# Performance work log

Hardware: AMD Instinct MI355X
Metric: run time of the kernel (lower is better)

## Reference

```python
import jax, jax.numpy as jnp
import numpy as np

B, T, D, H = 16, 2048, 512, 512  # batch, seq_len, input_dim, hidden_dim


def setup_inputs() -> dict:
    key = jax.random.key(0)
    k1, k2, k3 = jax.random.split(key, 3)
    x = jax.random.normal(k1, (B, T, D), dtype=jnp.float32)
    # vanilla tanh RnnCell parameters
    W_xh = jax.random.normal(k2, (D, H), dtype=jnp.float32) / np.float32(np.sqrt(D))
    W_hh = jax.random.normal(k3, (H, H), dtype=jnp.float32) / np.float32(np.sqrt(H))
    b = jnp.zeros((H,), dtype=jnp.float32)
    # DFA feedback matrix, 'diagonal' init branch: diag(linspace(0,1,H))
    A = jnp.diag(jnp.linspace(0.0, 1.0, H).astype(jnp.float32))
    return {"x": x, "W_xh": W_xh, "W_hh": W_hh, "b": b, "A": A}


def reference(x, W_xh, W_hh, b, A):
    # Forward of DfaRnn: sequential RNN loop. detach() does not change forward
    # values, so this is a plain tanh RNN scan. A only affects the backward.
    Bb = x.shape[0]
    h0 = jnp.zeros((Bb, W_hh.shape[0]), dtype=x.dtype)

    def step(h, xt):
        h_new = jnp.tanh(xt @ W_xh + h @ W_hh + b)
        return h_new, h_new

    _, hs = jax.lax.scan(step, h0, jnp.swapaxes(x, 0, 1))  # [T,B,H]
    return jnp.swapaxes(hs, 0, 1)  # [B,T,H]
```

## Files before the change

kernel.cpp:

```cpp
#include <hip/hip_runtime.h>
#include <cmath>

#define B_ 16
#define T_ 2048
#define D_ 512
#define H_ 512

__global__ __launch_bounds__(256) void gemm_xw(
    const float* __restrict__ x,
    const float* __restrict__ Wxh,
    const float* __restrict__ bias,
    float* __restrict__ out)
{
    const int tid = threadIdx.x;
    const int n0 = blockIdx.x * 128;
    const int m0 = blockIdx.y * 128;

    __shared__ float As[8][132];
    __shared__ float Bs[8][132];

    const int tx = tid & 15, ty = tid >> 4;
    float acc[8][8] = {};

    const int arow = tid >> 1;
    const int akq  = (tid & 1) * 4;
    const int brow = tid >> 5;
    const int bcol = (tid & 31) * 4;

    for (int k0 = 0; k0 < D_; k0 += 8) {
        float4 a4 = *(const float4*)(x + (size_t)(m0 + arow) * D_ + k0 + akq);
        float4 b4 = *(const float4*)(Wxh + (size_t)(k0 + brow) * H_ + n0 + bcol);
        __syncthreads();
        As[akq + 0][arow] = a4.x;
        As[akq + 1][arow] = a4.y;
        As[akq + 2][arow] = a4.z;
        As[akq + 3][arow] = a4.w;
        *(float4*)(&Bs[brow][bcol]) = b4;
        __syncthreads();
#pragma unroll
        for (int kk = 0; kk < 8; ++kk) {
            float4 a0 = *(const float4*)(&As[kk][ty * 8]);
            float4 a1 = *(const float4*)(&As[kk][ty * 8 + 4]);
            float4 b0 = *(const float4*)(&Bs[kk][tx * 8]);
            float4 b1 = *(const float4*)(&Bs[kk][tx * 8 + 4]);
            float a_[8] = {a0.x, a0.y, a0.z, a0.w, a1.x, a1.y, a1.z, a1.w};
            float b_[8] = {b0.x, b0.y, b0.z, b0.w, b1.x, b1.y, b1.z, b1.w};
#pragma unroll
            for (int i = 0; i < 8; ++i)
#pragma unroll
                for (int j = 0; j < 8; ++j) acc[i][j] += a_[i] * b_[j];
        }
    }

    const float4 bv0 = *(const float4*)(bias + n0 + tx * 8);
    const float4 bv1 = *(const float4*)(bias + n0 + tx * 8 + 4);
    const float bb[8] = {bv0.x, bv0.y, bv0.z, bv0.w, bv1.x, bv1.y, bv1.z, bv1.w};
#pragma unroll
    for (int i = 0; i < 8; ++i) {
        const int m = m0 + ty * 8 + i;
        float4 o0, o1;
        o0.x = acc[i][0] + bb[0]; o0.y = acc[i][1] + bb[1];
        o0.z = acc[i][2] + bb[2]; o0.w = acc[i][3] + bb[3];
        o1.x = acc[i][4] + bb[4]; o1.y = acc[i][5] + bb[5];
        o1.z = acc[i][6] + bb[6]; o1.w = acc[i][7] + bb[7];
        *(float4*)(out + (size_t)m * H_ + n0 + tx * 8)     = o0;
        *(float4*)(out + (size_t)m * H_ + n0 + tx * 8 + 4) = o1;
    }
}

__device__ __forceinline__ void bar_lds() {
    asm volatile("s_waitcnt lgkmcnt(0)\n\ts_barrier" ::: "memory");
}

__global__ __launch_bounds__(512, 2) void rnn_rec(
    const float* __restrict__ Whh,
    float* __restrict__ out,
    unsigned long long* __restrict__ ws)
{
    const int tid = threadIdx.x;
    const int b = blockIdx.x & 15;
    const int s = blockIdx.x >> 4;
    const int j = tid & 63;
    const int p = tid >> 6;
    const int col = (s << 6) + j;

    __shared__ float h_lds[H_];
    __shared__ float part[8 * 64];

    float W_reg[64];
    {
        const float* wbase = Whh + (size_t)(p * 64) * H_ + col;
#pragma unroll
        for (int r = 0; r < 64; ++r) {
            const float* addr = wbase + (size_t)r * H_;
            asm volatile("global_load_dword %0, %1, off"
                         : "=v"(W_reg[r]) : "v"(addr));
        }
        asm volatile("s_waitcnt vmcnt(0)" ::: "memory");
    }

    h_lds[tid] = 0.0f;
    __syncthreads();

    float* outb = out + (size_t)b * T_ * H_;
    unsigned long long* wsb = ws + (size_t)b * 2 * H_;

    float xw0 = 0.0f, xw1 = 0.0f, xw2 = 0.0f;
    if (p == 0) {
        xw0 = outb[(size_t)0 * H_ + col];
        xw1 = outb[(size_t)1 * H_ + col];
        xw2 = outb[(size_t)2 * H_ + col];
    }

    for (int t = 0; t < T_; ++t) {
        float acc = 0.0f;
        const float4* hv = (const float4*)(h_lds + (p << 6));
#pragma unroll
        for (int i = 0; i < 16; ++i) {
            float4 h4 = hv[i];
            acc += h4.x * W_reg[4 * i + 0];
            acc += h4.y * W_reg[4 * i + 1];
            acc += h4.z * W_reg[4 * i + 2];
            acc += h4.w * W_reg[4 * i + 3];
        }
        part[tid] = acc;
        bar_lds();

        const unsigned int tag = (unsigned int)(t + 1);
        const int slot = (t + 1) & 1;
        unsigned long long* wslot = wsb + (size_t)slot * H_;

        if (p == 0) {
            asm volatile("s_waitcnt vmcnt(0)" ::: "memory");
            float ssum = xw0;
#pragma unroll
            for (int q = 0; q < 8; ++q) ssum += part[q * 64 + j];
            union { unsigned int u; float f; } cv;
            cv.f = tanhf(ssum);
            unsigned long long pv =
                ((unsigned long long)tag << 32) | (unsigned long long)cv.u;
            __hip_atomic_store(wslot + col, pv, __ATOMIC_RELAXED,
                               __HIP_MEMORY_SCOPE_AGENT);
            outb[(size_t)t * H_ + col] = cv.f;
            h_lds[col] = cv.f;
            xw0 = xw1;
            xw1 = xw2;
            xw2 = (t + 3 < T_) ? outb[(size_t)(t + 3) * H_ + col] : 0.0f;
        } else {
            const int q = (p == s) ? 0 : p;
            unsigned long long* src = wslot + (q << 6) + j;
            unsigned long long v;
            do {
                v = __hip_atomic_load(src, __ATOMIC_RELAXED,
                                      __HIP_MEMORY_SCOPE_AGENT);
            } while ((unsigned int)(v >> 32) < tag);
            union { unsigned int u; float f; } cv;
            cv.u = (unsigned int)v;
            h_lds[(q << 6) + j] = cv.f;
        }
        bar_lds();
    }
}

extern "C" void kernel_launch(void* const* d_in, const int* in_sizes, int n_in,
                              void* d_out, int out_size, void* d_ws,
                              size_t ws_size, hipStream_t stream) {
    const float* x    = (const float*)d_in[0];
    const float* Wxh  = (const float*)d_in[1];
    const float* Whh  = (const float*)d_in[2];
    const float* bias = (const float*)d_in[3];
    float* out = (float*)d_out;

    hipMemsetAsync(d_ws, 0, (size_t)B_ * 2 * H_ * sizeof(unsigned long long),
                   stream);

    dim3 ggrid(H_ / 128, (B_ * T_) / 128, 1);
    gemm_xw<<<ggrid, 256, 0, stream>>>(x, Wxh, bias, out);

    rnn_rec<<<128, 512, 0, stream>>>(Whh, out, (unsigned long long*)d_ws);
}
```

Measured before the change: 2.973 ms.

## Add same-XCC fast path for cross-block hidden-state exchange via sc0 loads

Blocks record their XCC id in workspace. When producer and consumer slices sit on the same XCC, consumers poll a second mailbox with sc0-scoped loads that can hit the shared L2, and fall back to the agent-scope atomic mailbox on timeout. Producers write both mailboxes. This aims to cut the latency of the per-timestep inter-block handshake, at the cost of an extra store per step, a startup handshake, and reliance on cache-coherence behaviour that differs by scope.

```diff
diff --git a/kernel.cpp b/kernel.cpp
--- a/kernel.cpp
+++ b/kernel.cpp
@@ -68,6 +68,11 @@
     }
 }
 
+#define SLOW_OFF 0
+#define FAST_OFF (B_ * 2 * H_)
+#define HS_OFF   (B_ * 2 * H_ * 2)
+#define WS_U64   (B_ * 2 * H_ * 2 + B_ * 8)
+
 __device__ __forceinline__ void bar_lds() {
     asm volatile("s_waitcnt lgkmcnt(0)\n\ts_barrier" ::: "memory");
 }
@@ -75,7 +80,8 @@
 __global__ __launch_bounds__(512, 2) void rnn_rec(
     const float* __restrict__ Whh,
     float* __restrict__ out,
-    unsigned long long* __restrict__ ws)
+    unsigned long long* __restrict__ ws,
+    int use_fast)
 {
     const int tid = threadIdx.x;
     const int b = blockIdx.x & 15;
@@ -103,7 +109,33 @@
     __syncthreads();
 
     float* outb = out + (size_t)b * T_ * H_;
-    unsigned long long* wsb = ws + (size_t)b * 2 * H_;
+    unsigned long long* wsb_s = ws + SLOW_OFF + (size_t)b * 2 * H_;
+    unsigned long long* wsb_f = ws + FAST_OFF + (size_t)b * 2 * H_;
+    unsigned long long* hsb   = ws + HS_OFF + (size_t)b * 8;
+
+    const int q = (p == s) ? 0 : p;
+
+    bool fast = false;
+    if (use_fast) {
+        unsigned int my_xcc;
+        asm("s_getreg_b32 %0, hwreg(HW_REG_XCC_ID)" : "=s"(my_xcc));
+        my_xcc &= 0xF;
+        if (tid == 0) {
+            __hip_atomic_store(hsb + s,
+                               (1ull << 32) | (unsigned long long)my_xcc,
+                               __ATOMIC_RELAXED, __HIP_MEMORY_SCOPE_AGENT);
+        }
+        if (p != 0) {
+            unsigned long long hv = 0;
+            bool got = false;
+            for (int spin = 0; spin < (1 << 20); ++spin) {
+                hv = __hip_atomic_load(hsb + q, __ATOMIC_RELAXED,
+                                       __HIP_MEMORY_SCOPE_AGENT);
+                if ((unsigned int)(hv >> 32) >= 1u) { got = true; break; }
+            }
+            fast = got && (((unsigned int)hv & 0xF) == my_xcc);
+        }
+    }
 
     float xw0 = 0.0f, xw1 = 0.0f, xw2 = 0.0f;
     if (p == 0) {
@@ -114,10 +146,10 @@
 
     for (int t = 0; t < T_; ++t) {
         float acc = 0.0f;
-        const float4* hv = (const float4*)(h_lds + (p << 6));
+        const float4* hv4 = (const float4*)(h_lds + (p << 6));
 #pragma unroll
         for (int i = 0; i < 16; ++i) {
-            float4 h4 = hv[i];
+            float4 h4 = hv4[i];
             acc += h4.x * W_reg[4 * i + 0];
             acc += h4.y * W_reg[4 * i + 1];
             acc += h4.z * W_reg[4 * i + 2];
@@ -128,18 +160,23 @@
 
         const unsigned int tag = (unsigned int)(t + 1);
         const int slot = (t + 1) & 1;
-        unsigned long long* wslot = wsb + (size_t)slot * H_;
+        unsigned long long* wslot_s = wsb_s + (size_t)slot * H_;
+        unsigned long long* wslot_f = wsb_f + (size_t)slot * H_;
 
         if (p == 0) {
             asm volatile("s_waitcnt vmcnt(0)" ::: "memory");
             float ssum = xw0;
 #pragma unroll
-            for (int q = 0; q < 8; ++q) ssum += part[q * 64 + j];
+            for (int qq = 0; qq < 8; ++qq) ssum += part[qq * 64 + j];
             union { unsigned int u; float f; } cv;
             cv.f = tanhf(ssum);
             unsigned long long pv =
                 ((unsigned long long)tag << 32) | (unsigned long long)cv.u;
-            __hip_atomic_store(wslot + col, pv, __ATOMIC_RELAXED,
+            if (use_fast) {
+                asm volatile("global_store_dwordx2 %0, %1, off"
+                             :: "v"(wslot_f + col), "v"(pv) : "memory");
+            }
+            __hip_atomic_store(wslot_s + col, pv, __ATOMIC_RELAXED,
                                __HIP_MEMORY_SCOPE_AGENT);
             outb[(size_t)t * H_ + col] = cv.f;
             h_lds[col] = cv.f;
@@ -147,13 +184,29 @@
             xw1 = xw2;
             xw2 = (t + 3 < T_) ? outb[(size_t)(t + 3) * H_ + col] : 0.0f;
         } else {
-            const int q = (p == s) ? 0 : p;
-            unsigned long long* src = wslot + (q << 6) + j;
-            unsigned long long v;
-            do {
-                v = __hip_atomic_load(src, __ATOMIC_RELAXED,
-                                      __HIP_MEMORY_SCOPE_AGENT);
-            } while ((unsigned int)(v >> 32) < tag);
+            unsigned long long v = 0;
+            bool have = false;
+            if (fast) {
+                unsigned long long* src = wslot_f + (q << 6) + j;
+                for (int spin = 0; spin < 16384; ++spin) {
+                    asm volatile(
+                        "global_load_dwordx2 %0, %1, off sc0\n\t"
+                        "s_waitcnt vmcnt(0)"
+                        : "=v"(v) : "v"(src) : "memory");
+                    if (__all((unsigned int)(v >> 32) >= tag)) {
+                        have = true;
+                        break;
+                    }
+                }
+                if (!have) fast = false;
+            }
+            if (!have) {
+                unsigned long long* src = wslot_s + (q << 6) + j;
+                do {
+                    v = __hip_atomic_load(src, __ATOMIC_RELAXED,
+                                          __HIP_MEMORY_SCOPE_AGENT);
+                } while ((unsigned int)(v >> 32) < tag);
+            }
             union { unsigned int u; float f; } cv;
             cv.u = (unsigned int)v;
             h_lds[(q << 6) + j] = cv.f;
@@ -171,11 +224,14 @@
     const float* bias = (const float*)d_in[3];
     float* out = (float*)d_out;
 
-    hipMemsetAsync(d_ws, 0, (size_t)B_ * 2 * H_ * sizeof(unsigned long long),
-                   stream);
+    const size_t need_fast = (size_t)WS_U64 * sizeof(unsigned long long);
+    const size_t need_slow = (size_t)(B_ * 2 * H_) * sizeof(unsigned long long);
+    const int use_fast = (ws_size >= need_fast) ? 1 : 0;
+    hipMemsetAsync(d_ws, 0, use_fast ? need_fast : need_slow, stream);
 
     dim3 ggrid(H_ / 128, (B_ * T_) / 128, 1);
     gemm_xw<<<ggrid, 256, 0, stream>>>(x, Wxh, bias, out);
 
-    rnn_rec<<<128, 512, 0, stream>>>(Whh, out, (unsigned long long*)d_ws);
-}
+    rnn_rec<<<128, 512, 0, stream>>>(Whh, out, (unsigned long long*)d_ws,
+                                     use_fast);
+}
```

Result: slower. 7.505 ms (+152.4%).
